# Performance work log

Measured on AMD Instinct MI355X. Metric: run time of the kernel, lower is better.

The kernel has to match this reference:

```python
import jax, jax.numpy as jnp
import numpy as np

B, T, E, H = 2, 384, 768, 12
HD = E // H  # 64


def setup_inputs() -> dict:
    key = jax.random.key(0)
    ks = jax.random.split(key, 12)
    s = 0.02  # init scale
    inp = {
        "hidden_states": jax.random.normal(ks[0], (B, T, E), dtype=jnp.float32),
        # Linear weights stored as [in, out] so forward is x @ W + b
        "Wq": jax.random.normal(ks[1], (E, E), dtype=jnp.float32) * s,
        "bq": jnp.zeros((E,), dtype=jnp.float32),
        "Wk": jax.random.normal(ks[2], (E, E), dtype=jnp.float32) * s,
        "bk": jnp.zeros((E,), dtype=jnp.float32),
        "Wv": jax.random.normal(ks[3], (E, E), dtype=jnp.float32) * s,
        "bv": jnp.zeros((E,), dtype=jnp.float32),
        "Wo": jax.random.normal(ks[4], (E, E), dtype=jnp.float32) * s,
        "bo": jnp.zeros((E,), dtype=jnp.float32),
        # score_proj: Linear(head_dim, 1)
        "w_score": jax.random.normal(ks[5], (HD,), dtype=jnp.float32) * s,
        "b_score": jnp.zeros((1,), dtype=jnp.float32),
    }
    return inp


def reference(hidden_states, Wq, bq, Wk, bk, Wv, bv, Wo, bo, w_score, b_score):
    bsz, tgt_len, embed_dim = hidden_states.shape
    num_heads = H
    head_dim = embed_dim // num_heads

    def shape_heads(x):  # [B, L, E] -> [B, H, L, hd]
        return x.reshape(bsz, -1, num_heads, head_dim).transpose(0, 2, 1, 3)

    q = shape_heads(hidden_states @ Wq + bq)  # [B,H,T,hd]
    k = shape_heads(hidden_states @ Wk + bk)  # [B,H,S,hd]
    v = shape_heads(hidden_states @ Wv + bv)  # [B,H,S,hd]

    # additive (Bahdanau) score: score_proj(tanh(q_t + k_s)) -> [B,H,T,S]
    feat = jnp.tanh(q[:, :, :, None, :] + k[:, :, None, :, :])  # [B,H,T,S,hd]
    score = jnp.einsum("bhtsd,d->bhts", feat, w_score) + b_score[0]

    p_attn = jax.nn.softmax(score, axis=-1)                      # [B,H,T,S]
    attn = jnp.einsum("bhts,bhsd->bhtd", p_attn, v)              # [B,H,T,hd]

    attn = attn.transpose(0, 2, 1, 3).reshape(bsz, tgt_len, embed_dim)
    return attn @ Wo + bo
```

## Files before the change

### kernel.cpp

```cpp
#include <hip/hip_runtime.h>

#define Bc 2
#define Tc 384
#define Ec 768
#define Hc 12
#define HDc 64
#define TTc 8
#define SCc 64
#define SSPLIT 2
#define SHALF (Tc / SSPLIT)
#define NCHUNK (SHALF / SCc)
#define BHT (Bc * Hc * Tc)

typedef __attribute__((ext_vector_type(8))) short short8;
typedef __attribute__((ext_vector_type(4))) float f32x4;

#define CCONST 2.8853900817779268f

__device__ __forceinline__ float fexp2(float x) { return __builtin_amdgcn_exp2f(x); }
__device__ __forceinline__ float frcp(float x)  { return __builtin_amdgcn_rcpf(x); }

__device__ __forceinline__ unsigned short bf16_rne(float x) {
    unsigned u = __float_as_uint(x);
    u += 0x7fffu + ((u >> 16) & 1u);
    return (unsigned short)(u >> 16);
}
__device__ __forceinline__ float bf16_to_f(unsigned short h) {
    return __uint_as_float(((unsigned)h) << 16);
}

__global__ __launch_bounds__(256) void prep_kernel(
    const float* __restrict__ hs,
    const float* __restrict__ Wq, const float* __restrict__ Wk,
    const float* __restrict__ Wv, const float* __restrict__ Wo,
    unsigned short* __restrict__ hs_hi,
    unsigned short* __restrict__ wt_hi, unsigned short* __restrict__ wt_lo)
{
    const int tid = threadIdx.x;
    int id = blockIdx.x;
    if (id < 144) {
        int base = id * 4096 + tid * 16;
#pragma unroll
        for (int i = 0; i < 4; ++i) {
            float4 x = *reinterpret_cast<const float4*>(&hs[base + i * 4]);
            ushort4 hv;
            hv.x = bf16_rne(x.x);
            hv.y = bf16_rne(x.y);
            hv.z = bf16_rne(x.z);
            hv.w = bf16_rne(x.w);
            *reinterpret_cast<ushort4*>(&hs_hi[base + i * 4]) = hv;
        }
    } else {
        id -= 144;
        const int w = id / 144, t = id % 144;
        const int tr = t / 12, tc2 = t % 12;
        const float* W = (w == 0) ? Wq : (w == 1) ? Wk : (w == 2) ? Wv : Wo;
        unsigned short* TH = wt_hi + (size_t)w * Ec * Ec;
        unsigned short* TL = wt_lo + (size_t)w * Ec * Ec;

        __shared__ float tile[64][68];
        const int r = tid >> 2, c0 = (tid & 3) * 16;
#pragma unroll
        for (int i = 0; i < 4; ++i)
            *reinterpret_cast<float4*>(&tile[r][c0 + i * 4]) =
                *reinterpret_cast<const float4*>(&W[(tr * 64 + r) * Ec + tc2 * 64 + c0 + i * 4]);
        __syncthreads();
        const int n = tid >> 2, k0 = (tid & 3) * 4;
#pragma unroll
        for (int i = 0; i < 4; ++i) {
            int k = k0 + i * 16;
            float v0 = tile[k + 0][n], v1 = tile[k + 1][n];
            float v2 = tile[k + 2][n], v3 = tile[k + 3][n];
            ushort4 hv;
            hv.x = bf16_rne(v0);
            hv.y = bf16_rne(v1);
            hv.z = bf16_rne(v2);
            hv.w = bf16_rne(v3);
            size_t off = (size_t)(tc2 * 64 + n) * Ec + tr * 64 + k;
            *reinterpret_cast<ushort4*>(&TH[off]) = hv;
            if (w == 3) {
                ushort4 lv;
                lv.x = bf16_rne(v0 - bf16_to_f(hv.x));
                lv.y = bf16_rne(v1 - bf16_to_f(hv.y));
                lv.z = bf16_rne(v2 - bf16_to_f(hv.z));
                lv.w = bf16_rne(v3 - bf16_to_f(hv.w));
                *reinterpret_cast<ushort4*>(&TL[off]) = lv;
            }
        }
    }
}

__global__ __launch_bounds__(256) void gemm_qkv(
    const unsigned short* __restrict__ Ahi,
    const unsigned short* __restrict__ Bh0,
    const unsigned short* __restrict__ Bh1,
    const unsigned short* __restrict__ Bh2,
    const float* __restrict__ b0, const float* __restrict__ b1, const float* __restrict__ b2,
    float* __restrict__ C0, float* __restrict__ C1,
    unsigned short* __restrict__ Vt)
{
    const int z = blockIdx.z;
    const unsigned short* Bhi = (z == 0) ? Bh0 : (z == 1) ? Bh1 : Bh2;
    const float* bias = (z == 0) ? b0 : (z == 1) ? b1 : b2;

    __shared__ __align__(16) short sAh[64][72], sBh[64][72];

    const int tid = threadIdx.x;
    const int m0 = blockIdx.y * 64, n0 = blockIdx.x * 64;
    const int wave = tid >> 6, lane = tid & 63;
    const int wm = (wave >> 1) * 32, wn = (wave & 1) * 32;
    const int fr = lane & 15, fk = (lane >> 4) * 8;
    const int sr = tid >> 3, sg = (tid & 7) * 8;

    f32x4 zero = {0.f, 0.f, 0.f, 0.f};
    f32x4 acc[2][2];
    acc[0][0] = zero; acc[0][1] = zero; acc[1][0] = zero; acc[1][1] = zero;

    for (int kc = 0; kc < Ec; kc += 64) {
        int4 a0 = *reinterpret_cast<const int4*>(&Ahi[(size_t)(m0 + sr) * Ec + kc + sg]);
        int4 a1 = *reinterpret_cast<const int4*>(&Ahi[(size_t)(m0 + sr + 32) * Ec + kc + sg]);
        int4 w0 = *reinterpret_cast<const int4*>(&Bhi[(size_t)(n0 + sr) * Ec + kc + sg]);
        int4 w1 = *reinterpret_cast<const int4*>(&Bhi[(size_t)(n0 + sr + 32) * Ec + kc + sg]);
        __syncthreads();
        *reinterpret_cast<int4*>(&sAh[sr][sg])      = a0;
        *reinterpret_cast<int4*>(&sAh[sr + 32][sg]) = a1;
        *reinterpret_cast<int4*>(&sBh[sr][sg])      = w0;
        *reinterpret_cast<int4*>(&sBh[sr + 32][sg]) = w1;
        __syncthreads();

#pragma unroll
        for (int ks = 0; ks < 64; ks += 32) {
            short8 ah[2], bh[2];
#pragma unroll
            for (int mi = 0; mi < 2; ++mi)
                ah[mi] = *reinterpret_cast<const short8*>(&sAh[wm + mi * 16 + fr][ks + fk]);
#pragma unroll
            for (int ni = 0; ni < 2; ++ni)
                bh[ni] = *reinterpret_cast<const short8*>(&sBh[wn + ni * 16 + fr][ks + fk]);
#pragma unroll
            for (int mi = 0; mi < 2; ++mi)
#pragma unroll
                for (int ni = 0; ni < 2; ++ni)
                    acc[mi][ni] = __builtin_amdgcn_mfma_f32_16x16x32_bf16(ah[mi], bh[ni], acc[mi][ni], 0, 0, 0);
        }
        __syncthreads();
    }

    const int rbase = (lane >> 4) * 4;
#pragma unroll
    for (int ni = 0; ni < 2; ++ni) {
        const int cn = n0 + wn + ni * 16 + fr;
        const float bsv = bias[cn];
#pragma unroll
        for (int mi = 0; mi < 2; ++mi) {
            const int rm = m0 + wm + mi * 16 + rbase;
            if (z == 2) {
                const int bb = rm / Tc, ss = rm % Tc;
                const int hh = cn >> 6, dd = cn & 63;
                ushort4 pk;
                pk.x = bf16_rne(acc[mi][ni][0] + bsv);
                pk.y = bf16_rne(acc[mi][ni][1] + bsv);
                pk.z = bf16_rne(acc[mi][ni][2] + bsv);
                pk.w = bf16_rne(acc[mi][ni][3] + bsv);
                *reinterpret_cast<ushort4*>(
                    &Vt[((size_t)(bb * Hc + hh) * HDc + dd) * Tc + ss]) = pk;
            } else {
                float* C = (z == 0) ? C0 : C1;
#pragma unroll
                for (int rr = 0; rr < 4; ++rr)
                    C[(size_t)(rm + rr) * Ec + cn] = fexp2((acc[mi][ni][rr] + bsv) * CCONST);
            }
        }
    }
}

__global__ __launch_bounds__(256) void gemm_out(
    const unsigned short* __restrict__ Ahi, const unsigned short* __restrict__ Alo,
    const unsigned short* __restrict__ Bhi, const unsigned short* __restrict__ Blo,
    const float* __restrict__ bias_p,
    float* __restrict__ C0)
{
    __shared__ __align__(16) short sAh[64][72], sAl[64][72], sBh[64][72], sBl[64][72];

    const int tid = threadIdx.x;
    const int m0 = blockIdx.y * 64, n0 = blockIdx.x * 64;
    const int wave = tid >> 6, lane = tid & 63;
    const int wm = (wave >> 1) * 32, wn = (wave & 1) * 32;
    const int fr = lane & 15, fk = (lane >> 4) * 8;
    const int sr = tid >> 3, sg = (tid & 7) * 8;

    f32x4 zero = {0.f, 0.f, 0.f, 0.f};
    f32x4 acc[2][2];
    acc[0][0] = zero; acc[0][1] = zero; acc[1][0] = zero; acc[1][1] = zero;

    for (int kc = 0; kc < Ec; kc += 64) {
        int4 a0 = *reinterpret_cast<const int4*>(&Ahi[(size_t)(m0 + sr) * Ec + kc + sg]);
        int4 a1 = *reinterpret_cast<const int4*>(&Ahi[(size_t)(m0 + sr + 32) * Ec + kc + sg]);
        int4 a2 = *reinterpret_cast<const int4*>(&Alo[(size_t)(m0 + sr) * Ec + kc + sg]);
        int4 a3 = *reinterpret_cast<const int4*>(&Alo[(size_t)(m0 + sr + 32) * Ec + kc + sg]);
        int4 w0 = *reinterpret_cast<const int4*>(&Bhi[(size_t)(n0 + sr) * Ec + kc + sg]);
        int4 w1 = *reinterpret_cast<const int4*>(&Bhi[(size_t)(n0 + sr + 32) * Ec + kc + sg]);
        int4 w2 = *reinterpret_cast<const int4*>(&Blo[(size_t)(n0 + sr) * Ec + kc + sg]);
        int4 w3 = *reinterpret_cast<const int4*>(&Blo[(size_t)(n0 + sr + 32) * Ec + kc + sg]);
        __syncthreads();
        *reinterpret_cast<int4*>(&sAh[sr][sg])      = a0;
        *reinterpret_cast<int4*>(&sAh[sr + 32][sg]) = a1;
        *reinterpret_cast<int4*>(&sAl[sr][sg])      = a2;
        *reinterpret_cast<int4*>(&sAl[sr + 32][sg]) = a3;
        *reinterpret_cast<int4*>(&sBh[sr][sg])      = w0;
        *reinterpret_cast<int4*>(&sBh[sr + 32][sg]) = w1;
        *reinterpret_cast<int4*>(&sBl[sr][sg])      = w2;
        *reinterpret_cast<int4*>(&sBl[sr + 32][sg]) = w3;
        __syncthreads();

#pragma unroll
        for (int ks = 0; ks < 64; ks += 32) {
            short8 ah[2], al[2], bh[2], bl[2];
#pragma unroll
            for (int mi = 0; mi < 2; ++mi) {
                ah[mi] = *reinterpret_cast<const short8*>(&sAh[wm + mi * 16 + fr][ks + fk]);
                al[mi] = *reinterpret_cast<const short8*>(&sAl[wm + mi * 16 + fr][ks + fk]);
            }
#pragma unroll
            for (int ni = 0; ni < 2; ++ni) {
                bh[ni] = *reinterpret_cast<const short8*>(&sBh[wn + ni * 16 + fr][ks + fk]);
                bl[ni] = *reinterpret_cast<const short8*>(&sBl[wn + ni * 16 + fr][ks + fk]);
            }
#pragma unroll
            for (int mi = 0; mi < 2; ++mi)
#pragma unroll
                for (int ni = 0; ni < 2; ++ni) {
                    acc[mi][ni] = __builtin_amdgcn_mfma_f32_16x16x32_bf16(ah[mi], bh[ni], acc[mi][ni], 0, 0, 0);
                    acc[mi][ni] = __builtin_amdgcn_mfma_f32_16x16x32_bf16(ah[mi], bl[ni], acc[mi][ni], 0, 0, 0);
                    acc[mi][ni] = __builtin_amdgcn_mfma_f32_16x16x32_bf16(al[mi], bh[ni], acc[mi][ni], 0, 0, 0);
                }
        }
        __syncthreads();
    }

    const int rbase = (lane >> 4) * 4;
#pragma unroll
    for (int ni = 0; ni < 2; ++ni) {
        const int cn = n0 + wn + ni * 16 + fr;
        const float bsv = bias_p[cn];
#pragma unroll
        for (int mi = 0; mi < 2; ++mi) {
            const int rm = m0 + wm + mi * 16 + rbase;
#pragma unroll
            for (int rr = 0; rr < 4; ++rr)
                C0[(size_t)(rm + rr) * Ec + cn] = acc[mi][ni][rr] + bsv;
        }
    }
}

__global__ __launch_bounds__(256) void score_softmax_kernel(
    const float* __restrict__ EQ, const float* __restrict__ EK,
    const float* __restrict__ w_score,
    unsigned short* __restrict__ Pg, float* __restrict__ Rpart)
{
    const int bh = blockIdx.x;
    const int b = bh / Hc, h = bh % Hc;
    const int t0 = blockIdx.y * TTc;
    const int sbase = blockIdx.z * SHALF;
    const int tid = threadIdx.x;
    const int wave = tid >> 6, lane = tid & 63;

    __shared__ float qs[TTc][HDc];
    __shared__ float kv[SCc][HDc + 4];

    {
        int r = tid >> 5, d2 = (tid & 31) << 1;
        float2 qv = *reinterpret_cast<const float2*>(
            &EQ[(size_t)(b * Tc + t0 + r) * Ec + h * HDc + d2]);
        qs[r][d2] = qv.x;
        qs[r][d2 + 1] = qv.y;
    }
    __syncthreads();

    const int ta = wave, tb = wave + 4;
    unsigned short* dstA = &Pg[((size_t)bh * Tc + t0 + ta) * Tc + sbase + lane];
    unsigned short* dstB = &Pg[((size_t)bh * Tc + t0 + tb) * Tc + sbase + lane];

    float sum0 = 0.f, sum1 = 0.f;

    for (int c = 0; c < NCHUNK; ++c) {
        const int s0 = sbase + c * SCc;
        if (c > 0) __syncthreads();
#pragma unroll
        for (int i = 0; i < 4; ++i) {
            int id = i * 256 + tid;
            int srr = id >> 4, d4 = (id & 15) << 2;
            float4 kvv = *reinterpret_cast<const float4*>(
                &EK[(size_t)(b * Tc + s0 + srr) * Ec + h * HDc + d4]);
            *reinterpret_cast<float4*>(&kv[srr][d4]) = kvv;
        }
        __syncthreads();
        float a0 = 0.f, a1 = 0.f;
#pragma unroll
        for (int d4 = 0; d4 < HDc; d4 += 4) {
            float4 k4 = *reinterpret_cast<const float4*>(&kv[lane][d4]);
            float4 qa = *reinterpret_cast<const float4*>(&qs[ta][d4]);
            float4 qb = *reinterpret_cast<const float4*>(&qs[tb][d4]);
            a0 = fmaf(w_score[d4 + 0], frcp(fmaf(qa.x, k4.x, 1.f)), a0);
            a0 = fmaf(w_score[d4 + 1], frcp(fmaf(qa.y, k4.y, 1.f)), a0);
            a0 = fmaf(w_score[d4 + 2], frcp(fmaf(qa.z, k4.z, 1.f)), a0);
            a0 = fmaf(w_score[d4 + 3], frcp(fmaf(qa.w, k4.w, 1.f)), a0);
            a1 = fmaf(w_score[d4 + 0], frcp(fmaf(qb.x, k4.x, 1.f)), a1);
            a1 = fmaf(w_score[d4 + 1], frcp(fmaf(qb.y, k4.y, 1.f)), a1);
            a1 = fmaf(w_score[d4 + 2], frcp(fmaf(qb.z, k4.z, 1.f)), a1);
            a1 = fmaf(w_score[d4 + 3], frcp(fmaf(qb.w, k4.w, 1.f)), a1);
        }
        float p0 = fexp2(-a0 * CCONST);
        float p1 = fexp2(-a1 * CCONST);
        dstA[c * SCc] = bf16_rne(p0);
        dstB[c * SCc] = bf16_rne(p1);
        sum0 += p0;
        sum1 += p1;
    }

#pragma unroll
    for (int off = 32; off > 0; off >>= 1) {
        sum0 += __shfl_xor(sum0, off, 64);
        sum1 += __shfl_xor(sum1, off, 64);
    }
    if (lane == 0) {
        Rpart[(size_t)blockIdx.z * BHT + bh * Tc + t0 + ta] = sum0;
        Rpart[(size_t)blockIdx.z * BHT + bh * Tc + t0 + tb] = sum1;
    }
}

__global__ __launch_bounds__(256) void pv_mfma(
    const unsigned short* __restrict__ Pg, const unsigned short* __restrict__ Vt,
    const float* __restrict__ Rpart,
    unsigned short* __restrict__ Ohi, unsigned short* __restrict__ Olo)
{
    const int bh = blockIdx.x;
    const int b = bh / Hc, h = bh % Hc;
    const int tt = blockIdx.y;
    const int tid = threadIdx.x;
    const int wave = tid >> 6, lane = tid & 63;
    const int fr = lane & 15, fk = (lane >> 4) * 8;

    const unsigned short* Pbase = Pg + ((size_t)bh * Tc + tt * 64 + wave * 16 + fr) * Tc + fk;
    const unsigned short* Vbase = Vt + (size_t)bh * HDc * Tc + fk;

    f32x4 zero = {0.f, 0.f, 0.f, 0.f};
    f32x4 acc[4];
    acc[0] = zero; acc[1] = zero; acc[2] = zero; acc[3] = zero;

    for (int ks = 0; ks < Tc; ks += 32) {
        short8 af = *reinterpret_cast<const short8*>(Pbase + ks);
#pragma unroll
        for (int ni = 0; ni < 4; ++ni) {
            short8 bf = *reinterpret_cast<const short8*>(
                Vbase + (size_t)(ni * 16 + fr) * Tc + ks);
            acc[ni] = __builtin_amdgcn_mfma_f32_16x16x32_bf16(af, bf, acc[ni], 0, 0, 0);
        }
    }

    const int rbase = (lane >> 4) * 4;
    float rv[4];
#pragma unroll
    for (int rr = 0; rr < 4; ++rr) {
        size_t ridx = (size_t)bh * Tc + tt * 64 + wave * 16 + rbase + rr;
        rv[rr] = frcp(Rpart[ridx] + Rpart[ridx + BHT]);
    }

#pragma unroll
    for (int ni = 0; ni < 4; ++ni) {
#pragma unroll
        for (int rr = 0; rr < 4; ++rr) {
            int t_out = tt * 64 + wave * 16 + rbase + rr;
            float x = acc[ni][rr] * rv[rr];
            unsigned short hb = bf16_rne(x);
            unsigned short lb = bf16_rne(x - bf16_to_f(hb));
            size_t idx = (size_t)(b * Tc + t_out) * Ec + h * HDc + ni * 16 + fr;
            Ohi[idx] = hb;
            Olo[idx] = lb;
        }
    }
}

extern "C" void kernel_launch(void* const* d_in, const int* in_sizes, int n_in,
                              void* d_out, int out_size, void* d_ws, size_t ws_size,
                              hipStream_t stream) {
    const float* hs  = (const float*)d_in[0];
    const float* Wq  = (const float*)d_in[1];
    const float* bq  = (const float*)d_in[2];
    const float* Wk  = (const float*)d_in[3];
    const float* bk  = (const float*)d_in[4];
    const float* Wv  = (const float*)d_in[5];
    const float* bv  = (const float*)d_in[6];
    const float* Wo  = (const float*)d_in[7];
    const float* bo  = (const float*)d_in[8];
    const float* wsc = (const float*)d_in[9];
    float* out = (float*)d_out;

    const size_t MAT = (size_t)(Bc * Tc) * Ec;
    const size_t PSZ = (size_t)Bc * Hc * Tc * Tc;
    float* EQw = (float*)d_ws;
    float* EKw = EQw + MAT;
    float* Rpart = EKw + MAT;
    unsigned short* Vt    = (unsigned short*)(Rpart + 2 * (size_t)BHT);
    unsigned short* Pgb   = Vt + MAT;
    unsigned short* HS_HI = Pgb + PSZ;
    unsigned short* HS_LO = HS_HI + MAT;
    unsigned short* WT_HI = HS_LO + MAT;
    unsigned short* WT_LO = WT_HI + 4 * MAT;

    prep_kernel<<<720, 256, 0, stream>>>(hs, Wq, Wk, Wv, Wo, HS_HI, WT_HI, WT_LO);

    gemm_qkv<<<dim3(Ec / 64, (Bc * Tc) / 64, 3), 256, 0, stream>>>(
        HS_HI,
        WT_HI + 0 * MAT, WT_HI + 1 * MAT, WT_HI + 2 * MAT,
        bq, bk, bv, EQw, EKw, Vt);

    score_softmax_kernel<<<dim3(Bc * Hc, Tc / TTc, SSPLIT), 256, 0, stream>>>(
        EQw, EKw, wsc, Pgb, Rpart);

    pv_mfma<<<dim3(Bc * Hc, Tc / 64), 256, 0, stream>>>(Pgb, Vt, Rpart, HS_HI, HS_LO);

    gemm_out<<<dim3(Ec / 64, (Bc * Tc) / 64, 1), 256, 0, stream>>>(
        HS_HI, HS_LO,
        WT_HI + 3 * MAT, WT_LO + 3 * MAT,
        bo, out);
}
```

Before: 75.50 us.

## Split output GEMM along K and split score kernel keys three ways

The output projection GEMM now runs with a split-K of two. Each half writes its partial sums into the reused EQ/EK workspace, and a new elementwise kernel adds the two partials plus the bias. The score/softmax kernel now splits the key dimension three ways instead of two, and pv sums three partial row-sum buffers. Both changes aim to launch more blocks on the many CUs of the MI355X. In exchange they cost an extra kernel launch, extra global traffic for the partials, and smaller per-block work.

```diff
diff --git a/kernel.cpp b/kernel.cpp
--- a/kernel.cpp
+++ b/kernel.cpp
@@ -7,7 +7,7 @@
 #define HDc 64
 #define TTc 8
 #define SCc 64
-#define SSPLIT 2
+#define SSPLIT 3
 #define SHALF (Tc / SSPLIT)
 #define NCHUNK (SHALF / SCc)
 #define BHT (Bc * Hc * Tc)
@@ -177,13 +177,13 @@
 __global__ __launch_bounds__(256) void gemm_out(
     const unsigned short* __restrict__ Ahi, const unsigned short* __restrict__ Alo,
     const unsigned short* __restrict__ Bhi, const unsigned short* __restrict__ Blo,
-    const float* __restrict__ bias_p,
-    float* __restrict__ C0)
+    float* __restrict__ Cp)
 {
     __shared__ __align__(16) short sAh[64][72], sAl[64][72], sBh[64][72], sBl[64][72];
 
     const int tid = threadIdx.x;
     const int m0 = blockIdx.y * 64, n0 = blockIdx.x * 64;
+    const int kc0 = blockIdx.z * (Ec / 2);
     const int wave = tid >> 6, lane = tid & 63;
     const int wm = (wave >> 1) * 32, wn = (wave & 1) * 32;
     const int fr = lane & 15, fk = (lane >> 4) * 8;
@@ -193,7 +193,7 @@
     f32x4 acc[2][2];
     acc[0][0] = zero; acc[0][1] = zero; acc[1][0] = zero; acc[1][1] = zero;
 
-    for (int kc = 0; kc < Ec; kc += 64) {
+    for (int kc = kc0; kc < kc0 + Ec / 2; kc += 64) {
         int4 a0 = *reinterpret_cast<const int4*>(&Ahi[(size_t)(m0 + sr) * Ec + kc + sg]);
         int4 a1 = *reinterpret_cast<const int4*>(&Ahi[(size_t)(m0 + sr + 32) * Ec + kc + sg]);
         int4 a2 = *reinterpret_cast<const int4*>(&Alo[(size_t)(m0 + sr) * Ec + kc + sg]);
@@ -238,19 +238,36 @@
         __syncthreads();
     }
 
+    float* C = Cp + (size_t)blockIdx.z * (size_t)(Bc * Tc) * Ec;
     const int rbase = (lane >> 4) * 4;
 #pragma unroll
     for (int ni = 0; ni < 2; ++ni) {
         const int cn = n0 + wn + ni * 16 + fr;
-        const float bsv = bias_p[cn];
 #pragma unroll
         for (int mi = 0; mi < 2; ++mi) {
             const int rm = m0 + wm + mi * 16 + rbase;
 #pragma unroll
             for (int rr = 0; rr < 4; ++rr)
-                C0[(size_t)(rm + rr) * Ec + cn] = acc[mi][ni][rr] + bsv;
-        }
-    }
+                C[(size_t)(rm + rr) * Ec + cn] = acc[mi][ni][rr];
+        }
+    }
+}
+
+__global__ __launch_bounds__(256) void addbias_kernel(
+    const float* __restrict__ Cp, const float* __restrict__ bias,
+    float* __restrict__ out)
+{
+    const size_t MAT = (size_t)(Bc * Tc) * Ec;
+    int i = blockIdx.x * 1024 + threadIdx.x * 4;
+    float4 a = *reinterpret_cast<const float4*>(&Cp[i]);
+    float4 b = *reinterpret_cast<const float4*>(&Cp[MAT + i]);
+    float4 bs = *reinterpret_cast<const float4*>(&bias[i % Ec]);
+    float4 r;
+    r.x = a.x + b.x + bs.x;
+    r.y = a.y + b.y + bs.y;
+    r.z = a.z + b.z + bs.z;
+    r.w = a.w + b.w + bs.w;
+    *reinterpret_cast<float4*>(&out[i]) = r;
 }
 
 __global__ __launch_bounds__(256) void score_softmax_kernel(
@@ -363,7 +380,7 @@
 #pragma unroll
     for (int rr = 0; rr < 4; ++rr) {
         size_t ridx = (size_t)bh * Tc + tt * 64 + wave * 16 + rbase + rr;
-        rv[rr] = frcp(Rpart[ridx] + Rpart[ridx + BHT]);
+        rv[rr] = frcp(Rpart[ridx] + Rpart[ridx + BHT] + Rpart[ridx + 2 * BHT]);
     }
 
 #pragma unroll
@@ -401,7 +418,7 @@
     float* EQw = (float*)d_ws;
     float* EKw = EQw + MAT;
     float* Rpart = EKw + MAT;
-    unsigned short* Vt    = (unsigned short*)(Rpart + 2 * (size_t)BHT);
+    unsigned short* Vt    = (unsigned short*)(Rpart + 3 * (size_t)BHT);
     unsigned short* Pgb   = Vt + MAT;
     unsigned short* HS_HI = Pgb + PSZ;
     unsigned short* HS_LO = HS_HI + MAT;
@@ -420,8 +437,10 @@
 
     pv_mfma<<<dim3(Bc * Hc, Tc / 64), 256, 0, stream>>>(Pgb, Vt, Rpart, HS_HI, HS_LO);
 
-    gemm_out<<<dim3(Ec / 64, (Bc * Tc) / 64, 1), 256, 0, stream>>>(
+    gemm_out<<<dim3(Ec / 64, (Bc * Tc) / 64, 2), 256, 0, stream>>>(
         HS_HI, HS_LO,
         WT_HI + 3 * MAT, WT_LO + 3 * MAT,
-        bo, out);
-}
+        EQw);
+
+    addbias_kernel<<<(int)(MAT / 1024), 256, 0, stream>>>(EQw, bo, out);
+}
```

After: 73.60 us (median of 2 runs). 1.03x faster.
